# Performance work log

Hardware: AMD Instinct MI355X
Metric: run time of the kernel (lower is better)

## Reference

```python
import jax, jax.numpy as jnp
import numpy as np

C = 5.0          # tanh clamp constant (args.c, non-trainable)
B, N, R, D = 4, 16, 64, 256  # batch, block_num, block_len, word_dim
NEG = -1e9


def setup_inputs() -> dict:
    key = jax.random.key(0)
    ks = iter(jax.random.split(key, 80))

    def W(i, o):
        # xavier-like init (torch stores (out,in); we store (in,out) and use x @ W)
        return jax.random.normal(next(ks), (i, o), jnp.float32) * np.float32(np.sqrt(2.0 / (i + o)))

    def bvec(d):
        return jax.random.normal(next(ks), (d,), jnp.float32) * 0.01

    inp = {"x": jax.random.normal(next(ks), (B, N, R, D), jnp.float32)}
    for p in ("fw", "bw"):
        inp[f"fcW_{p}"] = W(D, D);  inp[f"fcb_{p}"] = bvec(D)
        inp[f"mW1_{p}"] = W(D, D);  inp[f"mW2_{p}"] = W(D, D);  inp[f"mb_{p}"] = bvec(D)
        inp[f"s2tW1_{p}"] = W(D, D); inp[f"s2tb1_{p}"] = bvec(D)
        inp[f"s2tW_{p}"] = W(D, D);  inp[f"s2tb_{p}"] = bvec(D)
        inp[f"gW1_{p}"] = W(D, D);  inp[f"gW2_{p}"] = W(D, D);  inp[f"gb_{p}"] = bvec(D)
        inp[f"fW1_{p}"] = W(3 * D, D); inp[f"fb1_{p}"] = bvec(D)
        inp[f"fW2_{p}"] = W(3 * D, D); inp[f"fb2_{p}"] = bvec(D)
    return inp


def _mSA(x, W1, W2, b, fw):
    # x: (..., L, d) -> (..., L, d). Additive per-feature attention with strict
    # triangular mask. fw: token i attends to j > i (last row zeroed);
    # bw: token i attends to j < i (first row zeroed). Matches the torch
    # -inf mask + narrow + zero-pad construction exactly.
    L = x.shape[-2]
    xi = (x @ W1)[..., :, None, :]                 # (..., L, 1, d)
    xj = (x @ W2)[..., None, :, :]                 # (..., 1, L, d)
    f = C * jnp.tanh((xi + xj + b) / C)            # (..., i, j, d)
    i = jnp.arange(L)[:, None]
    j = jnp.arange(L)[None, :]
    allowed = (j > i) if fw else (j < i)           # (L, L)
    scores = jnp.where(allowed[..., None], f, NEG)
    att = jax.nn.softmax(scores, axis=-2)          # softmax over j
    rowvalid = (jnp.arange(L) < L - 1) if fw else (jnp.arange(L) > 0)
    att = att * rowvalid[:, None, None].astype(x.dtype)
    return jnp.einsum('...ijd,...jd->...id', att, x)


def _s2t(x, W1, b1, Wo, bo):
    # source2token self-attention: (..., L, d) -> (..., d)
    f = jax.nn.relu(x @ W1 + b1)
    a = jax.nn.softmax(f @ Wo + bo, axis=-2)
    return jnp.sum(a * x, axis=-2)


def _mblosa(x, mW1, mW2, mb, s2tW1, s2tb1, s2tW, s2tb,
            gW1, gW2, gb, fW1, fb1, fW2, fb2, fw):
    Bb, n, r, d = x.shape
    h = _mSA(x, mW1, mW2, mb, fw)                  # (B, n, r, d) intra-block
    v = _s2t(h, s2tW1, s2tb1, s2tW, s2tb)          # (B, n, d)    block summary
    o = _mSA(v, mW1, mW2, mb, fw)                  # (B, n, d)    inter-block
    G = jax.nn.sigmoid(o @ gW1 + v @ gW2 + gb)
    e = G * o + (1.0 - G) * v                      # (B, n, d)
    # torch: cat of e[i] repeated r times, then narrow(1, 0, n)
    idx = jnp.arange(n) // r
    E = e[:, idx]                                  # (B, n, d)
    # torch: flatten blocks then narrow(1, 0, n) (faithful to source)
    xf = x.reshape(Bb, n * r, d)[:, :n]
    hf = h.reshape(Bb, n * r, d)[:, :n]
    cat = jnp.concatenate([xf, hf, E], axis=-1)    # (B, n, 3d)
    fusion = jax.nn.relu(cat @ fW1 + fb1)
    Gf = jax.nn.sigmoid(cat @ fW2 + fb2)
    return Gf * fusion + (1.0 - Gf) * xf           # (B, n, d)


def reference(x,
              fcW_fw, fcb_fw, mW1_fw, mW2_fw, mb_fw, s2tW1_fw, s2tb1_fw,
              s2tW_fw, s2tb_fw, gW1_fw, gW2_fw, gb_fw, fW1_fw, fb1_fw,
              fW2_fw, fb2_fw,
              fcW_bw, fcb_bw, mW1_bw, mW2_bw, mb_bw, s2tW1_bw, s2tb1_bw,
              s2tW_bw, s2tb_bw, gW1_bw, gW2_bw, gb_bw, fW1_bw, fb1_bw,
              fW2_bw, fb2_bw):
    in_fw = jax.nn.relu(x @ fcW_fw + fcb_fw)
    in_bw = jax.nn.relu(x @ fcW_bw + fcb_bw)
    u_fw = _mblosa(in_fw, mW1_fw, mW2_fw, mb_fw, s2tW1_fw, s2tb1_fw,
                   s2tW_fw, s2tb_fw, gW1_fw, gW2_fw, gb_fw,
                   fW1_fw, fb1_fw, fW2_fw, fb2_fw, True)
    u_bw = _mblosa(in_bw, mW1_bw, mW2_bw, mb_bw, s2tW1_bw, s2tb1_bw,
                   s2tW_bw, s2tb_bw, gW1_bw, gW2_bw, gb_bw,
                   fW1_bw, fb1_bw, fW2_bw, fb2_bw, False)
    return jnp.concatenate([u_fw, u_bw], axis=-1)  # (B, n, 2d)
```

## Files before the change

### kernel.cpp

```cpp
#include <hip/hip_runtime.h>
#include <hip/hip_bf16.h>

typedef __hip_bfloat16 BF16;
typedef __attribute__((ext_vector_type(8))) short short8;
typedef __attribute__((ext_vector_type(4))) short short4v;
typedef __attribute__((ext_vector_type(4))) float f32x4;

#define MFMA_B16(a,b,c) __builtin_amdgcn_mfma_f32_16x16x32_bf16((a),(b),(c),0,0,0)

#if __has_builtin(__builtin_amdgcn_exp2f)
#define EXP2F(x) __builtin_amdgcn_exp2f(x)
#else
#define EXP2F(x) __expf(0.6931471805599453f * (x))
#endif

__device__ __forceinline__ short f2bs(float f){ BF16 h = __float2bfloat16(f); return *(short*)&h; }
__device__ __forceinline__ float bs2f(short s){ BF16 h = *(BF16*)&s; return __bfloat162float(h); }

struct SrcPack { const float* s[10]; };

__global__ __launch_bounds__(256) void prep_k(SrcPack p, const float* __restrict__ X,
                                              short* __restrict__ Oh,
                                              short* __restrict__ Ol,
                                              short* __restrict__ Xh,
                                              short* __restrict__ Xl)
{
    if (blockIdx.y >= 10) {
        int u = (blockIdx.y - 10) * 16 + blockIdx.x;
        size_t base = (size_t)u * 16384;
        #pragma unroll
        for (int i = 0; i < 16; i++) {
            size_t idx = base + (size_t)i * 1024 + threadIdx.x * 4;
            float4 f = *(const float4*)(X + idx);
            short4v vh, vl;
            float t0[4] = {f.x, f.y, f.z, f.w};
            #pragma unroll
            for (int j = 0; j < 4; j++) {
                vh[j] = f2bs(t0[j]);
                vl[j] = f2bs(t0[j] - bs2f(vh[j]));
            }
            *(short4v*)(Xh + idx) = vh;
            *(short4v*)(Xl + idx) = vl;
        }
        return;
    }
    __shared__ float s[64][65];
    const float* W = p.s[blockIdx.y];
    short* oh = Oh + (size_t)blockIdx.y * 65536;
    short* ol = Ol + (size_t)blockIdx.y * 65536;
    int tr = (blockIdx.x >> 2) * 64, tc = (blockIdx.x & 3) * 64;
    #pragma unroll
    for (int i = 0; i < 16; i++) {
        int e = threadIdx.x + i * 256;
        int r = e >> 6, c = e & 63;
        s[c][r] = W[(size_t)(tr + r) * 256 + tc + c];
    }
    __syncthreads();
    #pragma unroll
    for (int i = 0; i < 16; i++) {
        int e = threadIdx.x + i * 256;
        int c2 = e >> 6, r2 = e & 63;
        float v = s[c2][r2];
        short hi = f2bs(v);
        short lo = f2bs(v - bs2f(hi));
        size_t oi = (size_t)(tc + c2) * 256 + tr + r2;
        oh[oi] = hi;
        ol[oi] = lo;
    }
}

template<int AM, int OM, int RELU, int BS>
__device__ __forceinline__ void gemm_body(const void* __restrict__ A0,
    const void* __restrict__ Alo,
    const short* __restrict__ Wh, const short* __restrict__ Wl,
    const float* __restrict__ bias, void* __restrict__ O0,
    int row0, int col0)
{
    constexpr int LDK = 72;
    __shared__ short sAh[64 * LDK];
    __shared__ short sAl[(AM == 0) ? 8 : 64 * LDK];
    __shared__ short sBh[64 * LDK];
    __shared__ short sBl[BS ? 8 : 64 * LDK];
    int tid = threadIdx.x;
    int w = tid >> 6, l = tid & 63;
    int m = l & 15, q = l >> 4;
    int sr = w * 16 + m;

    f32x4 acc[4];
    #pragma unroll
    for (int cf = 0; cf < 4; cf++) acc[cf] = (f32x4)(0.f);

    for (int kh = 0; kh < 4; kh++) {
        int kbase = kh * 64;
        #pragma unroll
        for (int i = 0; i < 2; i++) {
            int kl = q * 8 + 32 * i;
            size_t gofs = (size_t)(row0 + sr) * 256 + kbase + kl;
            if (AM == 2) {
                *(short8*)&sAh[sr * LDK + kl] = *(const short8*)((const short*)A0 + gofs);
                *(short8*)&sAl[sr * LDK + kl] = *(const short8*)((const short*)Alo + gofs);
            } else {
                *(short8*)&sAh[sr * LDK + kl] = *(const short8*)((const short*)A0 + gofs);
            }
            size_t gofsB = (size_t)(col0 + sr) * 256 + kbase + kl;
            *(short8*)&sBh[sr * LDK + kl] = *(const short8*)(Wh + gofsB);
            if (!BS)
                *(short8*)&sBl[sr * LDK + kl] = *(const short8*)(Wl + gofsB);
        }
        __syncthreads();
        #pragma unroll
        for (int ch = 0; ch < 2; ch++) {
            int k = ch * 32 + q * 8;
            short8 ah = *(const short8*)&sAh[(w * 16 + m) * LDK + k];
            short8 al = (AM != 0) ? *(const short8*)&sAl[(w * 16 + m) * LDK + k] : ah;
            #pragma unroll
            for (int cf = 0; cf < 4; cf++) {
                short8 bh = *(const short8*)&sBh[(cf * 16 + m) * LDK + k];
                acc[cf] = MFMA_B16(ah, bh, acc[cf]);
                if (!BS) {
                    short8 bl = *(const short8*)&sBl[(cf * 16 + m) * LDK + k];
                    acc[cf] = MFMA_B16(ah, bl, acc[cf]);
                }
                if (AM != 0)
                    acc[cf] = MFMA_B16(al, bh, acc[cf]);
            }
        }
        __syncthreads();
    }
    #pragma unroll
    for (int cf = 0; cf < 4; cf++) {
        int col = col0 + cf * 16 + m;
        float bv = bias ? bias[col] : 0.f;
        #pragma unroll
        for (int r = 0; r < 4; r++) {
            int row = row0 + w * 16 + q * 4 + r;
            float v = acc[cf][r] + bv;
            if (RELU) v = fmaxf(v, 0.f);
            size_t oi = (size_t)row * 256 + col;
            if (OM == 0) {
                ((float*)O0)[oi] = v;
            } else {
                ((short*)O0)[oi] = f2bs(v);
            }
        }
    }
}

struct GDir { const void* A0; const void* Al; const short* Wh; const short* Wl;
              const float* bias; void* O0; };

template<int AM, int OM, int RELU, int BS>
__global__ __launch_bounds__(256) void gemm_k(GDir p0, GDir p1)
{
    GDir p = blockIdx.z ? p1 : p0;
    gemm_body<AM, OM, RELU, BS>(p.A0, p.Al, p.Wh, p.Wl, p.bias, p.O0,
                                blockIdx.x * 64, blockIdx.y * 64);
}

struct MbloDir { const short* Ah;
                 const short* W1h; const short* W2h;
                 const float* mb; short* Hh; int fw; };

__global__ __launch_bounds__(512) void mblo_k(MbloDir p0, MbloDir p1)
{
    __shared__ char smraw[33536] __attribute__((aligned(16)));
    short* gAh  = (short*)smraw;
    short* gB1h = gAh + 4608;
    short* gB2h = gAh + 9216;
    float* aP   = (float*)smraw;
    unsigned int* aQX = (unsigned int*)(smraw + 16896);

    const float KLN = -0.06931471805599453f;

    MbloDir p = blockIdx.z ? p1 : p0;
    int tid = threadIdx.x;
    int w = tid >> 6, l = tid & 63;
    int m = l & 15, q = l >> 4;
    int rh = w >> 1;
    int cb = (w & 1) * 2;
    int bn = blockIdx.x >> 1, ipar = blockIdx.x & 1;
    int row0 = bn * 64, d0 = blockIdx.y * 64;
    int srow = tid >> 3;
    int skl  = (tid & 7) * 8;

    f32x4 acc1[2], acc2[2];
    #pragma unroll
    for (int cf = 0; cf < 2; cf++) { acc1[cf] = (f32x4)(0.f); acc2[cf] = (f32x4)(0.f); }

    for (int kh = 0; kh < 4; kh++) {
        int kbase = kh * 64;
        size_t ga = (size_t)(row0 + srow) * 256 + kbase + skl;
        *(short8*)&gAh[srow * 72 + skl] = *(const short8*)(p.Ah + ga);
        size_t gb = (size_t)(d0 + srow) * 256 + kbase + skl;
        *(short8*)&gB1h[srow * 72 + skl] = *(const short8*)(p.W1h + gb);
        *(short8*)&gB2h[srow * 72 + skl] = *(const short8*)(p.W2h + gb);
        __syncthreads();
        #pragma unroll
        for (int ch = 0; ch < 2; ch++) {
            int k = ch * 32 + q * 8;
            short8 ah = *(const short8*)&gAh[(rh * 16 + m) * 72 + k];
            #pragma unroll
            for (int cf = 0; cf < 2; cf++) {
                int bofs = ((cb + cf) * 16 + m) * 72 + k;
                short8 b1 = *(const short8*)&gB1h[bofs];
                acc1[cf] = MFMA_B16(ah, b1, acc1[cf]);
                short8 b2 = *(const short8*)&gB2h[bofs];
                acc2[cf] = MFMA_B16(ah, b2, acc2[cf]);
            }
        }
        __syncthreads();
    }
    short* sQX = (short*)aQX;
    #pragma unroll
    for (int cf = 0; cf < 2; cf++) {
        int col = (cb + cf) * 16 + m;
        float mbv = p.mb[d0 + col];
        #pragma unroll
        for (int r = 0; r < 4; r++) {
            int row = rh * 16 + q * 4 + r;
            aP[row * 66 + col] = __expf(0.4f * acc1[cf][r]) * KLN;
            sQX[col * 130 + 2 * row] = f2bs(__expf(0.4f * (acc2[cf][r] + mbv)));
        }
    }
    {
        size_t gx = (size_t)(row0 + srow) * 256 + d0 + skl;
        short8 xh = *(const short8*)(p.Ah + gx);
        #pragma unroll
        for (int t = 0; t < 8; t++)
            sQX[(skl + t) * 130 + 2 * srow + 1] = xh[t];
    }
    __syncthreads();
    const unsigned int* lane_qx = &aQX[l * 65];
    #pragma unroll
    for (int t8 = 0; t8 < 4; t8++) {
        int i = ipar + 2 * (w + 8 * t8);
        float Pp = aP[i * 66 + l];
        int js = p.fw ? (i + 1) : 0;
        int je = p.fw ? 64 : i;
        float den0 = 0.f, den1 = 0.f, num0 = 0.f, num1 = 0.f;
        int j = js;
        for (; j + 4 <= je; j += 4) {
            unsigned int u0 = lane_qx[j];
            unsigned int u1 = lane_qx[j + 1];
            unsigned int u2 = lane_qx[j + 2];
            unsigned int u3 = lane_qx[j + 3];
            float q0 = bs2f((short)(u0 & 0xffff)), x0 = bs2f((short)(u0 >> 16));
            float q1 = bs2f((short)(u1 & 0xffff)), x1 = bs2f((short)(u1 >> 16));
            float q2 = bs2f((short)(u2 & 0xffff)), x2 = bs2f((short)(u2 >> 16));
            float q3 = bs2f((short)(u3 & 0xffff)), x3 = bs2f((short)(u3 >> 16));
            float w0 = EXP2F(__builtin_amdgcn_rcpf(fmaf(Pp, q0, KLN)));
            float w1 = EXP2F(__builtin_amdgcn_rcpf(fmaf(Pp, q1, KLN)));
            float w2 = EXP2F(__builtin_amdgcn_rcpf(fmaf(Pp, q2, KLN)));
            float w3 = EXP2F(__builtin_amdgcn_rcpf(fmaf(Pp, q3, KLN)));
            den0 += w0; num0 = fmaf(w0, x0, num0);
            den1 += w1; num1 = fmaf(w1, x1, num1);
            den0 += w2; num0 = fmaf(w2, x2, num0);
            den1 += w3; num1 = fmaf(w3, x3, num1);
        }
        for (; j < je; j++) {
            unsigned int u0 = lane_qx[j];
            float q0 = bs2f((short)(u0 & 0xffff)), x0 = bs2f((short)(u0 >> 16));
            float wgt = EXP2F(__builtin_amdgcn_rcpf(fmaf(Pp, q0, KLN)));
            den0 += wgt; num0 = fmaf(wgt, x0, num0);
        }
        float den = den0 + den1, num = num0 + num1;
        bool valid = p.fw ? (i < 63) : (i > 0);
        float out = valid ? (num * __builtin_amdgcn_rcpf(den)) : 0.f;
        p.Hh[(size_t)(row0 + i) * 256 + d0 + l] = f2bs(out);
    }
}

struct PoolDir { const short* T1; const short* Wh; const float* bias;
                 const short* Hh; float* V; };

__global__ __launch_bounds__(256) void s2t_pool_k(PoolDir p0, PoolDir p1)
{
    __shared__ char smraw[37888] __attribute__((aligned(16)));
    short* gAh = (short*)smraw;
    short* gBh = gAh + 4608;
    float* aL = (float*)smraw;
    float* aH = aL + 4352;
    float* rm = aL + 8704;
    float* rd = aL + 8960;
    float* rn = aL + 9216;

    PoolDir p = blockIdx.z ? p1 : p0;
    int tid = threadIdx.x;
    int w = tid >> 6, l = tid & 63;
    int m = l & 15, q = l >> 4;
    int sr = w * 16 + m;
    int row0 = blockIdx.x * 64, d0 = blockIdx.y * 64;

    f32x4 acc[4];
    #pragma unroll
    for (int cf = 0; cf < 4; cf++) acc[cf] = (f32x4)(0.f);

    for (int kh = 0; kh < 4; kh++) {
        int kbase = kh * 64;
        #pragma unroll
        for (int i = 0; i < 2; i++) {
            int kl = q * 8 + 32 * i;
            *(short8*)&gAh[sr * 72 + kl] =
                *(const short8*)(p.T1 + (size_t)(row0 + sr) * 256 + kbase + kl);
            *(short8*)&gBh[sr * 72 + kl] =
                *(const short8*)(p.Wh + (size_t)(d0 + sr) * 256 + kbase + kl);
        }
        __syncthreads();
        #pragma unroll
        for (int ch = 0; ch < 2; ch++) {
            int k = ch * 32 + q * 8;
            short8 ah = *(const short8*)&gAh[(w * 16 + m) * 72 + k];
            #pragma unroll
            for (int cf = 0; cf < 4; cf++) {
                short8 bh = *(const short8*)&gBh[(cf * 16 + m) * 72 + k];
                acc[cf] = MFMA_B16(ah, bh, acc[cf]);
            }
        }
        __syncthreads();
    }
    #pragma unroll
    for (int cf = 0; cf < 4; cf++) {
        int col = cf * 16 + m;
        float bv = p.bias[d0 + col];
        #pragma unroll
        for (int r = 0; r < 4; r++) {
            int row = w * 16 + q * 4 + r;
            aL[row * 68 + col] = acc[cf][r] + bv;
        }
    }
    #pragma unroll
    for (int it = 0; it < 2; it++) {
        int e = tid + it * 256;
        int j = e >> 3, d8 = (e & 7) * 8;
        short8 xh = *(const short8*)(p.Hh + (size_t)(row0 + j) * 256 + d0 + d8);
        #pragma unroll
        for (int t = 0; t < 8; t++)
            aH[j * 68 + d8 + t] = bs2f(xh[t]);
    }
    __syncthreads();
    int dl = tid & 63, rq = tid >> 6;
    float mx = -1e30f, den = 0.f, num = 0.f;
    #pragma unroll
    for (int rr = 0; rr < 16; rr++) {
        int r = rq * 16 + rr;
        float lv = aL[r * 68 + dl];
        float hv = aH[r * 68 + dl];
        if (lv > mx) {
            float sc = __expf(mx - lv);
            den *= sc; num *= sc; mx = lv;
        }
        float wgt = __expf(lv - mx);
        den += wgt; num += wgt * hv;
    }
    rm[rq * 64 + dl] = mx; rd[rq * 64 + dl] = den; rn[rq * 64 + dl] = num;
    __syncthreads();
    if (rq == 0) {
        float M = fmaxf(fmaxf(rm[dl], rm[64 + dl]), fmaxf(rm[128 + dl], rm[192 + dl]));
        float D = 0.f, Nn = 0.f;
        #pragma unroll
        for (int k = 0; k < 4; k++) {
            float sc = __expf(rm[k * 64 + dl] - M);
            D += rd[k * 64 + dl] * sc;
            Nn += rn[k * 64 + dl] * sc;
        }
        p.V[(size_t)blockIdx.x * 256 + d0 + dl] = Nn / D;
    }
}

struct Gate2Dir { const float* V; const float* W1; const float* W2; const float* mb;
                  const float* gW1; const float* gW2; const float* gb;
                  float* E0; int fw; };

__global__ __launch_bounds__(512) void attn2gate_k(Gate2Dir p0, Gate2Dir p1)
{
    Gate2Dir p = blockIdx.z ? p1 : p0;
    __shared__ __attribute__((aligned(16))) float sVT[4096];
    __shared__ float sPart[16][256];
    __shared__ float so[256], sv[256], red[8][64];
    int tid = threadIdx.x;
    int b = blockIdx.x;
    int k = tid & 255, half = tid >> 8;

    if (p.fw) {
        #pragma unroll
        for (int it = 0; it < 8; it++) {
            int e = tid + it * 512;
            int kk = e >> 4, j = e & 15;
            sVT[e] = p.V[(size_t)(b * 16 + j) * 256 + kk];
        }
        __syncthreads();
        float acc[16];
        #pragma unroll
        for (int j = 0; j < 16; j++) acc[j] = 0.f;
        int kk0 = half * 128;
        #pragma unroll 4
        for (int kk = kk0; kk < kk0 + 128; kk++) {
            const float4* vr = (const float4*)&sVT[kk * 16];
            float4 va = vr[0], vb = vr[1], vc = vr[2], vd = vr[3];
            float w1 = p.W1[(size_t)kk * 256 + k];
            float w2 = p.W2[(size_t)kk * 256 + k];
            acc[0]  = fmaf(va.x, w1, acc[0]);
            acc[1]  = fmaf(va.y, w2, acc[1]);
            acc[2]  = fmaf(va.z, w2, acc[2]);
            acc[3]  = fmaf(va.w, w2, acc[3]);
            acc[4]  = fmaf(vb.x, w2, acc[4]);
            acc[5]  = fmaf(vb.y, w2, acc[5]);
            acc[6]  = fmaf(vb.z, w2, acc[6]);
            acc[7]  = fmaf(vb.w, w2, acc[7]);
            acc[8]  = fmaf(vc.x, w2, acc[8]);
            acc[9]  = fmaf(vc.y, w2, acc[9]);
            acc[10] = fmaf(vc.z, w2, acc[10]);
            acc[11] = fmaf(vc.w, w2, acc[11]);
            acc[12] = fmaf(vd.x, w2, acc[12]);
            acc[13] = fmaf(vd.y, w2, acc[13]);
            acc[14] = fmaf(vd.z, w2, acc[14]);
            acc[15] = fmaf(vd.w, w2, acc[15]);
        }
        if (half) {
            #pragma unroll
            for (int j = 0; j < 16; j++) sPart[j][k] = acc[j];
        }
        __syncthreads();
        if (!half) {
            #pragma unroll
            for (int j = 0; j < 16; j++) acc[j] += sPart[j][k];
            float base = acc[0] + p.mb[k];
            float den = 0.f, num = 0.f;
            #pragma unroll
            for (int j = 1; j < 16; j++) {
                float z = (base + acc[j]) * 0.2f;
                float e2 = __expf(2.f * z);
                float t = 1.f - 2.f / (e2 + 1.f);
                float wgt = __expf(5.f * t);
                den += wgt;
                num = fmaf(wgt, p.V[(size_t)(b * 16 + j) * 256 + k], num);
            }
            so[k] = num / den;
            sv[k] = p.V[(size_t)(b * 16) * 256 + k];
        }
    } else {
        if (!half) {
            so[k] = 0.f;
            sv[k] = p.V[(size_t)(b * 16) * 256 + k];
        }
    }
    __syncthreads();
    int c = tid & 63, ks = tid >> 6;
    int gc = blockIdx.y * 64 + c;
    float a2 = 0.f;
    int k0 = ks * 32;
    #pragma unroll 8
    for (int kkx = 0; kkx < 32; kkx++) {
        int kx = k0 + kkx;
        a2 += so[kx] * p.gW1[(size_t)kx * 256 + gc] + sv[kx] * p.gW2[(size_t)kx * 256 + gc];
    }
    red[ks][c] = a2;
    __syncthreads();
    if (ks == 0) {
        float a = red[0][c] + red[1][c] + red[2][c] + red[3][c]
                + red[4][c] + red[5][c] + red[6][c] + red[7][c] + p.gb[gc];
        float G = 1.f / (1.f + __expf(-a));
        p.E0[b * 256 + gc] = G * so[gc] + (1.f - G) * sv[gc];
    }
}

struct FuseDir { const short* INh; const short* Hh;
                 const float* E0; const float* fW1; const float* fb1;
                 const float* fW2; const float* fb2; };

__global__ __launch_bounds__(256) void fusion_k(FuseDir p0, FuseDir p1, float* __restrict__ out)
{
    FuseDir p = blockIdx.z ? p1 : p0;
    __shared__ float cat[768];
    __shared__ float red1[4][64], red2[4][64];
    int bt = blockIdx.x, b = bt >> 4, t = bt & 15;
    int c = threadIdx.x & 63, ks = threadIdx.x >> 6;
    int gc = blockIdx.y * 64 + c;
    size_t xrow = ((size_t)b * 1024 + t) * 256;
    cat[threadIdx.x]       = bs2f(p.INh[xrow + threadIdx.x]);
    cat[256 + threadIdx.x] = bs2f(p.Hh[xrow + threadIdx.x]);
    cat[512 + threadIdx.x] = p.E0[b * 256 + threadIdx.x];
    __syncthreads();
    float a1 = 0.f, a2 = 0.f;
    int k0 = ks * 192;
    #pragma unroll 8
    for (int kk = 0; kk < 192; kk++) {
        int k = k0 + kk;
        float cv = cat[k];
        a1 += cv * p.fW1[(size_t)k * 256 + gc];
        a2 += cv * p.fW2[(size_t)k * 256 + gc];
    }
    red1[ks][c] = a1; red2[ks][c] = a2;
    __syncthreads();
    if (ks == 0) {
        float s1 = red1[0][c] + red1[1][c] + red1[2][c] + red1[3][c] + p.fb1[gc];
        float s2 = red2[0][c] + red2[1][c] + red2[2][c] + red2[3][c] + p.fb2[gc];
        float fus = fmaxf(s1, 0.f);
        float Gf = 1.f / (1.f + __expf(-s2));
        float u = Gf * fus + (1.f - Gf) * cat[gc];
        out[((size_t)(b * 16 + t)) * 512 + (size_t)blockIdx.z * 256 + gc] = u;
    }
}

extern "C" void kernel_launch(void* const* d_in, const int* in_sizes, int n_in,
                              void* d_out, int out_size, void* d_ws, size_t ws_size,
                              hipStream_t stream)
{
    const float* x = (const float*)d_in[0];
    char* base = (char*)d_ws;
    auto alloc = [&](size_t bytes){ void* r = base; base += (bytes + 255) & ~255ULL; return r; };
    short* inH = (short*)alloc(2 * 1048576 * 2);
    short* hH  = (short*)alloc(2 * 1048576 * 2);
    short* t1  = (short*)alloc(2 * 1048576 * 2);
    short* wtH = (short*)alloc(10 * 65536 * 2);
    short* wtL = (short*)alloc(10 * 65536 * 2);
    short* xh  = (short*)alloc(1048576 * 2);
    short* xl  = (short*)alloc(1048576 * 2);
    float* v   = (float*)alloc(2 * 16384 * 4);
    float* E0  = (float*)alloc(2 * 1024 * 4);

    SrcPack sp;
    const int src_idx[5] = {0, 2, 3, 5, 7};
    for (int p = 0; p < 2; p++)
        for (int i = 0; i < 5; i++)
            sp.s[p * 5 + i] = (const float*)d_in[1 + p * 16 + src_idx[i]];
    prep_k<<<dim3(16, 14), 256, 0, stream>>>(sp, x, wtH, wtL, xh, xl);

    GDir fc[2], s2t1[2];
    MbloDir mbd[2];
    PoolDir pld[2];
    Gate2Dir gtd[2];
    FuseDir fsd[2];
    for (int p = 0; p < 2; p++) {
        int bi = 1 + p * 16;
        const float* fcb   = (const float*)d_in[bi + 1];
        const float* mb    = (const float*)d_in[bi + 4];
        const float* s2tb1 = (const float*)d_in[bi + 6];
        const float* s2tb  = (const float*)d_in[bi + 8];
        size_t po = (size_t)p * 1048576;
        const short* W0h = wtH + (size_t)(p * 5 + 0) * 65536, *W0l = wtL + (size_t)(p * 5 + 0) * 65536;
        const short* W1h = wtH + (size_t)(p * 5 + 1) * 65536;
        const short* W2h = wtH + (size_t)(p * 5 + 2) * 65536;
        const short* W3h = wtH + (size_t)(p * 5 + 3) * 65536;
        const short* W4h = wtH + (size_t)(p * 5 + 4) * 65536;

        fc[p]   = { xh, xl, W0h, W0l, fcb, inH + po };
        mbd[p]  = { inH + po, W1h, W2h, mb, hH + po, (p == 0) };
        s2t1[p] = { hH + po, nullptr, W3h, nullptr, s2tb1, t1 + po };
        pld[p]  = { t1 + po, W4h, s2tb, hH + po, v + p * 16384 };
        gtd[p]  = { v + p * 16384,
                    (const float*)d_in[bi + 2], (const float*)d_in[bi + 3], mb,
                    (const float*)d_in[bi + 9], (const float*)d_in[bi + 10],
                    (const float*)d_in[bi + 11], E0 + p * 1024, (p == 0) };
        fsd[p]  = { inH + po, hH + po, E0 + p * 1024,
                    (const float*)d_in[bi + 12], (const float*)d_in[bi + 13],
                    (const float*)d_in[bi + 14], (const float*)d_in[bi + 15] };
    }

    gemm_k<2, 1, 1, 0><<<dim3(64, 4, 2), 256, 0, stream>>>(fc[0], fc[1]);
    mblo_k<<<dim3(128, 4, 2), 512, 0, stream>>>(mbd[0], mbd[1]);
    gemm_k<0, 1, 1, 1><<<dim3(64, 4, 2), 256, 0, stream>>>(s2t1[0], s2t1[1]);
    s2t_pool_k<<<dim3(64, 4, 2), 256, 0, stream>>>(pld[0], pld[1]);
    attn2gate_k<<<dim3(4, 4, 2), 512, 0, stream>>>(gtd[0], gtd[1]);
    fusion_k<<<dim3(64, 4, 2), 256, 0, stream>>>(fsd[0], fsd[1], (float*)d_out);
}
```

Before: 211.4 us.

## Fuse all stages into one cooperative persistent kernel with grid syncs

```diff
diff --git a/kernel.cpp b/kernel.cpp
--- a/kernel.cpp
+++ b/kernel.cpp
@@ -1,4 +1,5 @@
 #include <hip/hip_runtime.h>
+#include <hip/hip_cooperative_groups.h>
 #include <hip/hip_bf16.h>
 
 typedef __hip_bfloat16 BF16;
@@ -18,6 +19,19 @@
 __device__ __forceinline__ float bs2f(short s){ BF16 h = *(BF16*)&s; return __bfloat162float(h); }
 
 struct SrcPack { const float* s[10]; };
+struct GDir { const void* A0; const void* Al; const short* Wh; const short* Wl;
+              const float* bias; void* O0; };
+struct MbloDir { const short* Ah; const short* W1h; const short* W2h;
+                 const float* mb; short* Hh; int fw; };
+struct PoolDir { const short* T1; const short* Wh; const float* bias;
+                 const short* Hh; float* V; };
+struct Gate2Dir { const float* V; const float* W1; const float* W2; const float* mb;
+                  const float* gW1; const float* gW2; const float* gb;
+                  float* E0; int fw; };
+struct FuseDir { const short* INh; const short* Hh;
+                 const float* E0; const float* fW1; const float* fb1;
+                 const float* fW2; const float* fb2; };
+
 
 __global__ __launch_bounds__(256) void prep_k(SrcPack p, const float* __restrict__ X,
                                               short* __restrict__ Oh,
@@ -146,9 +160,6 @@
     }
 }
 
-struct GDir { const void* A0; const void* Al; const short* Wh; const short* Wl;
-              const float* bias; void* O0; };
-
 template<int AM, int OM, int RELU, int BS>
 __global__ __launch_bounds__(256) void gemm_k(GDir p0, GDir p1)
 {
@@ -156,10 +167,6 @@
     gemm_body<AM, OM, RELU, BS>(p.A0, p.Al, p.Wh, p.Wl, p.bias, p.O0,
                                 blockIdx.x * 64, blockIdx.y * 64);
 }
-
-struct MbloDir { const short* Ah;
-                 const short* W1h; const short* W2h;
-                 const float* mb; short* Hh; int fw; };
 
 __global__ __launch_bounds__(512) void mblo_k(MbloDir p0, MbloDir p1)
 {
@@ -270,9 +277,6 @@
     }
 }
 
-struct PoolDir { const short* T1; const short* Wh; const float* bias;
-                 const short* Hh; float* V; };
-
 __global__ __launch_bounds__(256) void s2t_pool_k(PoolDir p0, PoolDir p1)
 {
     __shared__ char smraw[37888] __attribute__((aligned(16)));
@@ -366,10 +370,6 @@
         p.V[(size_t)blockIdx.x * 256 + d0 + dl] = Nn / D;
     }
 }
-
-struct Gate2Dir { const float* V; const float* W1; const float* W2; const float* mb;
-                  const float* gW1; const float* gW2; const float* gb;
-                  float* E0; int fw; };
 
 __global__ __launch_bounds__(512) void attn2gate_k(Gate2Dir p0, Gate2Dir p1)
 {
@@ -464,10 +464,6 @@
     }
 }
 
-struct FuseDir { const short* INh; const short* Hh;
-                 const float* E0; const float* fW1; const float* fb1;
-                 const float* fW2; const float* fb2; };
-
 __global__ __launch_bounds__(256) void fusion_k(FuseDir p0, FuseDir p1, float* __restrict__ out)
 {
     FuseDir p = blockIdx.z ? p1 : p0;
@@ -502,6 +498,481 @@
     }
 }
 
+
+struct MegaP {
+    SrcPack sp; const float* X;
+    short *wtH, *wtL, *xh, *xl;
+    GDir fc[2], s2t1[2];
+    MbloDir mbd[2];
+    PoolDir pld[2];
+    Gate2Dir gtd[2];
+    FuseDir fsd[2];
+    float* out;
+};
+
+template<int AM, int OM, int RELU, int BS>
+__device__ __forceinline__ void gemm512(const void* __restrict__ A0,
+    const void* __restrict__ Alo,
+    const short* __restrict__ Wh, const short* __restrict__ Wl,
+    const float* __restrict__ bias, void* __restrict__ O0,
+    int row0, int col0, char* SM)
+{
+    short* sAh = (short*)SM;
+    short* sAl = (short*)(SM + 9216);
+    short* sBh = (short*)(SM + 18432);
+    short* sBl = (short*)(SM + 27648);
+    int tid = threadIdx.x;
+    int w = tid >> 6, l = tid & 63, m = l & 15, q = l >> 4;
+    int strip = w >> 1, chalf = w & 1;
+    int srow = tid >> 3, skl = (tid & 7) * 8;
+    f32x4 acc[2];
+    acc[0] = (f32x4)(0.f); acc[1] = (f32x4)(0.f);
+    for (int kh = 0; kh < 4; kh++) {
+        int kb = kh * 64;
+        size_t ga = (size_t)(row0 + srow) * 256 + kb + skl;
+        *(short8*)&sAh[srow * 72 + skl] = *(const short8*)((const short*)A0 + ga);
+        if (AM == 2)
+            *(short8*)&sAl[srow * 72 + skl] = *(const short8*)((const short*)Alo + ga);
+        size_t gb = (size_t)(col0 + srow) * 256 + kb + skl;
+        *(short8*)&sBh[srow * 72 + skl] = *(const short8*)(Wh + gb);
+        if (!BS)
+            *(short8*)&sBl[srow * 72 + skl] = *(const short8*)(Wl + gb);
+        __syncthreads();
+        #pragma unroll
+        for (int ch = 0; ch < 2; ch++) {
+            int k = ch * 32 + q * 8;
+            short8 ah = *(const short8*)&sAh[(strip * 16 + m) * 72 + k];
+            short8 al = (AM == 2) ? *(const short8*)&sAl[(strip * 16 + m) * 72 + k] : ah;
+            #pragma unroll
+            for (int cf = 0; cf < 2; cf++) {
+                int bofs = ((chalf * 2 + cf) * 16 + m) * 72 + k;
+                short8 bh = *(const short8*)&sBh[bofs];
+                acc[cf] = MFMA_B16(ah, bh, acc[cf]);
+                if (!BS) {
+                    short8 bl = *(const short8*)&sBl[bofs];
+                    acc[cf] = MFMA_B16(ah, bl, acc[cf]);
+                }
+                if (AM == 2)
+                    acc[cf] = MFMA_B16(al, bh, acc[cf]);
+            }
+        }
+        __syncthreads();
+    }
+    #pragma unroll
+    for (int cf = 0; cf < 2; cf++) {
+        int col = col0 + (chalf * 2 + cf) * 16 + m;
+        float bv = bias ? bias[col] : 0.f;
+        #pragma unroll
+        for (int r = 0; r < 4; r++) {
+            int row = row0 + strip * 16 + q * 4 + r;
+            float v = acc[cf][r] + bv;
+            if (RELU) v = fmaxf(v, 0.f);
+            size_t oi = (size_t)row * 256 + col;
+            if (OM == 0) ((float*)O0)[oi] = v;
+            else ((short*)O0)[oi] = f2bs(v);
+        }
+    }
+}
+
+__global__ __launch_bounds__(512) void mega_k(MegaP mp)
+{
+    __shared__ char SM[40960] __attribute__((aligned(16)));
+    cooperative_groups::grid_group gg = cooperative_groups::this_grid();
+    const int tid = threadIdx.x;
+    const int bid = blockIdx.x, nb = gridDim.x;
+    const float KLN = -0.06931471805599453f;
+
+    for (int job = bid; job < 224; job += nb) {
+        if (job < 160) {
+            int mat = job >> 4, tile = job & 15;
+            float (*s)[65] = (float(*)[65])SM;
+            const float* W = mp.sp.s[mat];
+            short* oh = mp.wtH + (size_t)mat * 65536;
+            short* ol = mp.wtL + (size_t)mat * 65536;
+            int tr = (tile >> 2) * 64, tc = (tile & 3) * 64;
+            #pragma unroll
+            for (int i = 0; i < 8; i++) {
+                int e = tid + i * 512;
+                int r = e >> 6, c = e & 63;
+                s[c][r] = W[(size_t)(tr + r) * 256 + tc + c];
+            }
+            __syncthreads();
+            #pragma unroll
+            for (int i = 0; i < 8; i++) {
+                int e = tid + i * 512;
+                int c2 = e >> 6, r2 = e & 63;
+                float v = s[c2][r2];
+                short hi = f2bs(v);
+                short lo = f2bs(v - bs2f(hi));
+                size_t oi = (size_t)(tc + c2) * 256 + tr + r2;
+                oh[oi] = hi;
+                ol[oi] = lo;
+            }
+            __syncthreads();
+        } else {
+            int u = job - 160;
+            size_t base = (size_t)u * 16384;
+            #pragma unroll
+            for (int i = 0; i < 8; i++) {
+                size_t idx = base + (size_t)i * 2048 + tid * 4;
+                float4 f = *(const float4*)(mp.X + idx);
+                short4v vh, vl;
+                float t0[4] = {f.x, f.y, f.z, f.w};
+                #pragma unroll
+                for (int j = 0; j < 4; j++) {
+                    vh[j] = f2bs(t0[j]);
+                    vl[j] = f2bs(t0[j] - bs2f(vh[j]));
+                }
+                *(short4v*)(mp.xh + idx) = vh;
+                *(short4v*)(mp.xl + idx) = vl;
+            }
+        }
+    }
+    gg.sync();
+
+    for (int job = bid; job < 512; job += nb) {
+        int dir = job >> 8, rem = job & 255;
+        GDir p = mp.fc[dir];
+        gemm512<2, 1, 1, 0>(p.A0, p.Al, p.Wh, p.Wl, p.bias, p.O0,
+                            (rem & 63) * 64, (rem >> 6) * 64, SM);
+    }
+    gg.sync();
+
+    {
+        short* gAh  = (short*)SM;
+        short* gB1h = gAh + 4608;
+        short* gB2h = gAh + 9216;
+        float* aP   = (float*)SM;
+        unsigned int* aQX = (unsigned int*)(SM + 16896);
+        int w = tid >> 6, l = tid & 63, m = l & 15, q = l >> 4;
+        int rh = w >> 1, cb = (w & 1) * 2;
+        int srow = tid >> 3, skl = (tid & 7) * 8;
+        for (int job = bid; job < 512; job += nb) {
+            int dir = job >> 8, rem = job & 255;
+            MbloDir p = mp.mbd[dir];
+            int row0 = (rem & 63) * 64, d0 = (rem >> 6) * 64;
+            f32x4 acc1[2], acc2[2];
+            #pragma unroll
+            for (int cf = 0; cf < 2; cf++) { acc1[cf] = (f32x4)(0.f); acc2[cf] = (f32x4)(0.f); }
+            for (int kh = 0; kh < 4; kh++) {
+                int kbase = kh * 64;
+                size_t ga = (size_t)(row0 + srow) * 256 + kbase + skl;
+                *(short8*)&gAh[srow * 72 + skl] = *(const short8*)(p.Ah + ga);
+                size_t gb = (size_t)(d0 + srow) * 256 + kbase + skl;
+                *(short8*)&gB1h[srow * 72 + skl] = *(const short8*)(p.W1h + gb);
+                *(short8*)&gB2h[srow * 72 + skl] = *(const short8*)(p.W2h + gb);
+                __syncthreads();
+                #pragma unroll
+                for (int ch = 0; ch < 2; ch++) {
+                    int k = ch * 32 + q * 8;
+                    short8 ah = *(const short8*)&gAh[(rh * 16 + m) * 72 + k];
+                    #pragma unroll
+                    for (int cf = 0; cf < 2; cf++) {
+                        int bofs = ((cb + cf) * 16 + m) * 72 + k;
+                        short8 b1 = *(const short8*)&gB1h[bofs];
+                        acc1[cf] = MFMA_B16(ah, b1, acc1[cf]);
+                        short8 b2 = *(const short8*)&gB2h[bofs];
+                        acc2[cf] = MFMA_B16(ah, b2, acc2[cf]);
+                    }
+                }
+                __syncthreads();
+            }
+            short* sQX = (short*)aQX;
+            #pragma unroll
+            for (int cf = 0; cf < 2; cf++) {
+                int col = (cb + cf) * 16 + m;
+                float mbv = p.mb[d0 + col];
+                #pragma unroll
+                for (int r = 0; r < 4; r++) {
+                    int row = rh * 16 + q * 4 + r;
+                    aP[row * 66 + col] = __expf(0.4f * acc1[cf][r]) * KLN;
+                    sQX[col * 130 + 2 * row] = f2bs(__expf(0.4f * (acc2[cf][r] + mbv)));
+                }
+            }
+            {
+                size_t gx = (size_t)(row0 + srow) * 256 + d0 + skl;
+                short8 xh = *(const short8*)(p.Ah + gx);
+                #pragma unroll
+                for (int t = 0; t < 8; t++)
+                    sQX[(skl + t) * 130 + 2 * srow + 1] = xh[t];
+            }
+            __syncthreads();
+            const unsigned int* lane_qx = &aQX[l * 65];
+            for (int t8 = 0; t8 < 8; t8++) {
+                int i = w + 8 * t8;
+                float Pp = aP[i * 66 + l];
+                int js = p.fw ? (i + 1) : 0;
+                int je = p.fw ? 64 : i;
+                float den0 = 0.f, den1 = 0.f, num0 = 0.f, num1 = 0.f;
+                int j = js;
+                for (; j + 4 <= je; j += 4) {
+                    unsigned int u0 = lane_qx[j];
+                    unsigned int u1 = lane_qx[j + 1];
+                    unsigned int u2 = lane_qx[j + 2];
+                    unsigned int u3 = lane_qx[j + 3];
+                    float q0 = bs2f((short)(u0 & 0xffff)), x0 = bs2f((short)(u0 >> 16));
+                    float q1 = bs2f((short)(u1 & 0xffff)), x1 = bs2f((short)(u1 >> 16));
+                    float q2 = bs2f((short)(u2 & 0xffff)), x2 = bs2f((short)(u2 >> 16));
+                    float q3 = bs2f((short)(u3 & 0xffff)), x3 = bs2f((short)(u3 >> 16));
+                    float w0 = EXP2F(__builtin_amdgcn_rcpf(fmaf(Pp, q0, KLN)));
+                    float w1 = EXP2F(__builtin_amdgcn_rcpf(fmaf(Pp, q1, KLN)));
+                    float w2 = EXP2F(__builtin_amdgcn_rcpf(fmaf(Pp, q2, KLN)));
+                    float w3 = EXP2F(__builtin_amdgcn_rcpf(fmaf(Pp, q3, KLN)));
+                    den0 += w0; num0 = fmaf(w0, x0, num0);
+                    den1 += w1; num1 = fmaf(w1, x1, num1);
+                    den0 += w2; num0 = fmaf(w2, x2, num0);
+                    den1 += w3; num1 = fmaf(w3, x3, num1);
+                }
+                for (; j < je; j++) {
+                    unsigned int u0 = lane_qx[j];
+                    float q0 = bs2f((short)(u0 & 0xffff)), x0 = bs2f((short)(u0 >> 16));
+                    float wgt = EXP2F(__builtin_amdgcn_rcpf(fmaf(Pp, q0, KLN)));
+                    den0 += wgt; num0 = fmaf(wgt, x0, num0);
+                }
+                float den = den0 + den1, num = num0 + num1;
+                bool valid = p.fw ? (i < 63) : (i > 0);
+                float out = valid ? (num * __builtin_amdgcn_rcpf(den)) : 0.f;
+                p.Hh[(size_t)(row0 + i) * 256 + d0 + l] = f2bs(out);
+            }
+            __syncthreads();
+        }
+    }
+    gg.sync();
+
+    for (int job = bid; job < 512; job += nb) {
+        int dir = job >> 8, rem = job & 255;
+        GDir p = mp.s2t1[dir];
+        gemm512<0, 1, 1, 1>(p.A0, nullptr, p.Wh, nullptr, p.bias, p.O0,
+                            (rem & 63) * 64, (rem >> 6) * 64, SM);
+    }
+    gg.sync();
+
+    {
+        short* gAh = (short*)SM;
+        short* gBh = gAh + 4608;
+        float* aL = (float*)SM;
+        float* aH = aL + 4352;
+        float* rm = (float*)(SM + 34816);
+        float* rd = rm + 512;
+        float* rn = rm + 1024;
+        int w = tid >> 6, l = tid & 63, m = l & 15, q = l >> 4;
+        int strip = w >> 1, chalf = w & 1;
+        int srow = tid >> 3, skl = (tid & 7) * 8;
+        for (int job = bid; job < 512; job += nb) {
+            int dir = job >> 8, rem = job & 255;
+            PoolDir p = mp.pld[dir];
+            int row0 = (rem & 63) * 64, d0 = (rem >> 6) * 64;
+            f32x4 acc[2];
+            acc[0] = (f32x4)(0.f); acc[1] = (f32x4)(0.f);
+            for (int kh = 0; kh < 4; kh++) {
+                int kbase = kh * 64;
+                *(short8*)&gAh[srow * 72 + skl] =
+                    *(const short8*)(p.T1 + (size_t)(row0 + srow) * 256 + kbase + skl);
+                *(short8*)&gBh[srow * 72 + skl] =
+                    *(const short8*)(p.Wh + (size_t)(d0 + srow) * 256 + kbase + skl);
+                __syncthreads();
+                #pragma unroll
+                for (int ch = 0; ch < 2; ch++) {
+                    int k = ch * 32 + q * 8;
+                    short8 ah = *(const short8*)&gAh[(strip * 16 + m) * 72 + k];
+                    #pragma unroll
+                    for (int cf = 0; cf < 2; cf++) {
+                        short8 bh = *(const short8*)&gBh[((chalf * 2 + cf) * 16 + m) * 72 + k];
+                        acc[cf] = MFMA_B16(ah, bh, acc[cf]);
+                    }
+                }
+                __syncthreads();
+            }
+            #pragma unroll
+            for (int cf = 0; cf < 2; cf++) {
+                int col = (chalf * 2 + cf) * 16 + m;
+                float bv = p.bias[d0 + col];
+                #pragma unroll
+                for (int r = 0; r < 4; r++) {
+                    int row = strip * 16 + q * 4 + r;
+                    aL[row * 68 + col] = acc[cf][r] + bv;
+                }
+            }
+            {
+                int j = tid >> 3, d8 = (tid & 7) * 8;
+                short8 xh = *(const short8*)(p.Hh + (size_t)(row0 + j) * 256 + d0 + d8);
+                #pragma unroll
+                for (int t = 0; t < 8; t++)
+                    aH[j * 68 + d8 + t] = bs2f(xh[t]);
+            }
+            __syncthreads();
+            int dl = tid & 63, rq = tid >> 6;
+            float mx = -1e30f, den = 0.f, num = 0.f;
+            #pragma unroll
+            for (int rr = 0; rr < 8; rr++) {
+                int r = rq * 8 + rr;
+                float lv = aL[r * 68 + dl];
+                float hv = aH[r * 68 + dl];
+                if (lv > mx) { float sc = __expf(mx - lv); den *= sc; num *= sc; mx = lv; }
+                float wgt = __expf(lv - mx);
+                den += wgt; num = fmaf(wgt, hv, num);
+            }
+            rm[rq * 64 + dl] = mx; rd[rq * 64 + dl] = den; rn[rq * 64 + dl] = num;
+            __syncthreads();
+            if (rq == 0) {
+                float M = rm[dl];
+                #pragma unroll
+                for (int kq = 1; kq < 8; kq++) M = fmaxf(M, rm[kq * 64 + dl]);
+                float D = 0.f, Nn = 0.f;
+                #pragma unroll
+                for (int kq = 0; kq < 8; kq++) {
+                    float sc = __expf(rm[kq * 64 + dl] - M);
+                    D += rd[kq * 64 + dl] * sc;
+                    Nn += rn[kq * 64 + dl] * sc;
+                }
+                p.V[(size_t)(rem & 63) * 256 + d0 + dl] = Nn / D;
+            }
+            __syncthreads();
+        }
+    }
+    gg.sync();
+
+    {
+        float* sVT = (float*)SM;
+        float (*sPart)[256] = (float(*)[256])(SM + 16384);
+        float* so = (float*)(SM + 32768);
+        float* sv = (float*)(SM + 33792);
+        float (*red)[64] = (float(*)[64])(SM + 34816);
+        for (int job = bid; job < 32; job += nb) {
+            int b = job & 3, gy = (job >> 2) & 3, dir = job >> 4;
+            Gate2Dir p = mp.gtd[dir];
+            int k = tid & 255, half = tid >> 8;
+            if (p.fw) {
+                #pragma unroll
+                for (int it = 0; it < 8; it++) {
+                    int e = tid + it * 512;
+                    int kk = e >> 4, j = e & 15;
+                    sVT[e] = p.V[(size_t)(b * 16 + j) * 256 + kk];
+                }
+                __syncthreads();
+                float acc[16];
+                #pragma unroll
+                for (int j = 0; j < 16; j++) acc[j] = 0.f;
+                int kk0 = half * 128;
+                #pragma unroll 4
+                for (int kk = kk0; kk < kk0 + 128; kk++) {
+                    const float4* vr = (const float4*)&sVT[kk * 16];
+                    float4 va = vr[0], vb = vr[1], vc = vr[2], vd = vr[3];
+                    float w1 = p.W1[(size_t)kk * 256 + k];
+                    float w2 = p.W2[(size_t)kk * 256 + k];
+                    acc[0]  = fmaf(va.x, w1, acc[0]);
+                    acc[1]  = fmaf(va.y, w2, acc[1]);
+                    acc[2]  = fmaf(va.z, w2, acc[2]);
+                    acc[3]  = fmaf(va.w, w2, acc[3]);
+                    acc[4]  = fmaf(vb.x, w2, acc[4]);
+                    acc[5]  = fmaf(vb.y, w2, acc[5]);
+                    acc[6]  = fmaf(vb.z, w2, acc[6]);
+                    acc[7]  = fmaf(vb.w, w2, acc[7]);
+                    acc[8]  = fmaf(vc.x, w2, acc[8]);
+                    acc[9]  = fmaf(vc.y, w2, acc[9]);
+                    acc[10] = fmaf(vc.z, w2, acc[10]);
+                    acc[11] = fmaf(vc.w, w2, acc[11]);
+                    acc[12] = fmaf(vd.x, w2, acc[12]);
+                    acc[13] = fmaf(vd.y, w2, acc[13]);
+                    acc[14] = fmaf(vd.z, w2, acc[14]);
+                    acc[15] = fmaf(vd.w, w2, acc[15]);
+                }
+                if (half) {
+                    #pragma unroll
+                    for (int j = 0; j < 16; j++) sPart[j][k] = acc[j];
+                }
+                __syncthreads();
+                if (!half) {
+                    #pragma unroll
+                    for (int j = 0; j < 16; j++) acc[j] += sPart[j][k];
+                    float base = acc[0] + p.mb[k];
+                    float den = 0.f, num = 0.f;
+                    #pragma unroll
+                    for (int j = 1; j < 16; j++) {
+                        float z = (base + acc[j]) * 0.2f;
+                        float e2 = __expf(2.f * z);
+                        float t = 1.f - 2.f / (e2 + 1.f);
+                        float wgt = __expf(5.f * t);
+                        den += wgt;
+                        num = fmaf(wgt, p.V[(size_t)(b * 16 + j) * 256 + k], num);
+                    }
+                    so[k] = num / den;
+                    sv[k] = p.V[(size_t)(b * 16) * 256 + k];
+                }
+            } else {
+                if (!half) {
+                    so[k] = 0.f;
+                    sv[k] = p.V[(size_t)(b * 16) * 256 + k];
+                }
+            }
+            __syncthreads();
+            int c = tid & 63, ks = tid >> 6;
+            int gc = gy * 64 + c;
+            float a2 = 0.f;
+            int k0 = ks * 32;
+            #pragma unroll 8
+            for (int kkx = 0; kkx < 32; kkx++) {
+                int kx = k0 + kkx;
+                a2 += so[kx] * p.gW1[(size_t)kx * 256 + gc] + sv[kx] * p.gW2[(size_t)kx * 256 + gc];
+            }
+            red[ks][c] = a2;
+            __syncthreads();
+            if (ks == 0) {
+                float a = red[0][c] + red[1][c] + red[2][c] + red[3][c]
+                        + red[4][c] + red[5][c] + red[6][c] + red[7][c] + p.gb[gc];
+                float G = 1.f / (1.f + __expf(-a));
+                p.E0[b * 256 + gc] = G * so[gc] + (1.f - G) * sv[gc];
+            }
+            __syncthreads();
+        }
+    }
+    gg.sync();
+
+    {
+        float* cat = (float*)SM;
+        float (*red1)[64] = (float(*)[64])(SM + 3072);
+        float (*red2)[64] = (float(*)[64])(SM + 5120);
+        for (int job = bid; job < 512; job += nb) {
+            int dir = job >> 8, rem = job & 255;
+            int bt = rem & 63, gy = rem >> 6;
+            FuseDir p = mp.fsd[dir];
+            int b = bt >> 4, t = bt & 15;
+            size_t xrow = ((size_t)b * 1024 + t) * 256;
+            if (tid < 256) {
+                cat[tid] = bs2f(p.INh[xrow + tid]);
+                cat[512 + tid] = p.E0[b * 256 + tid];
+            } else {
+                cat[tid] = bs2f(p.Hh[xrow + tid - 256]);
+            }
+            __syncthreads();
+            int c = tid & 63, ks = tid >> 6;
+            int gc = gy * 64 + c;
+            float a1 = 0.f, a2 = 0.f;
+            int k0 = ks * 96;
+            #pragma unroll 8
+            for (int kk = 0; kk < 96; kk++) {
+                int k = k0 + kk;
+                float cv = cat[k];
+                a1 += cv * p.fW1[(size_t)k * 256 + gc];
+                a2 += cv * p.fW2[(size_t)k * 256 + gc];
+            }
+            red1[ks][c] = a1; red2[ks][c] = a2;
+            __syncthreads();
+            if (ks == 0) {
+                float s1 = p.fb1[gc], s2 = p.fb2[gc];
+                #pragma unroll
+                for (int kq = 0; kq < 8; kq++) { s1 += red1[kq][c]; s2 += red2[kq][c]; }
+                float fus = fmaxf(s1, 0.f);
+                float Gf = 1.f / (1.f + __expf(-s2));
+                float u = Gf * fus + (1.f - Gf) * cat[gc];
+                mp.out[((size_t)(b * 16 + t)) * 512 + (size_t)dir * 256 + gc] = u;
+            }
+            __syncthreads();
+        }
+    }
+}
+
+
 extern "C" void kernel_launch(void* const* d_in, const int* in_sizes, int n_in,
                               void* d_out, int out_size, void* d_ws, size_t ws_size,
                               hipStream_t stream)
@@ -524,7 +995,6 @@
     for (int p = 0; p < 2; p++)
         for (int i = 0; i < 5; i++)
             sp.s[p * 5 + i] = (const float*)d_in[1 + p * 16 + src_idx[i]];
-    prep_k<<<dim3(16, 14), 256, 0, stream>>>(sp, x, wtH, wtL, xh, xl);
 
     GDir fc[2], s2t1[2];
     MbloDir mbd[2];
@@ -557,10 +1027,47 @@
                     (const float*)d_in[bi + 14], (const float*)d_in[bi + 15] };
     }
 
-    gemm_k<2, 1, 1, 0><<<dim3(64, 4, 2), 256, 0, stream>>>(fc[0], fc[1]);
-    mblo_k<<<dim3(128, 4, 2), 512, 0, stream>>>(mbd[0], mbd[1]);
-    gemm_k<0, 1, 1, 1><<<dim3(64, 4, 2), 256, 0, stream>>>(s2t1[0], s2t1[1]);
-    s2t_pool_k<<<dim3(64, 4, 2), 256, 0, stream>>>(pld[0], pld[1]);
-    attn2gate_k<<<dim3(4, 4, 2), 512, 0, stream>>>(gtd[0], gtd[1]);
-    fusion_k<<<dim3(64, 4, 2), 256, 0, stream>>>(fsd[0], fsd[1], (float*)d_out);
+    static int coopGrid = -2;
+    if (coopGrid == -2) {
+        int perCU = 0;
+        hipError_t e1 = hipOccupancyMaxActiveBlocksPerMultiprocessor(&perCU, mega_k, 512, 0);
+        if (e1 == hipSuccess && perCU > 0) {
+            hipDeviceProp_t prop;
+            int dev = 0;
+            hipGetDevice(&dev);
+            if (hipGetDeviceProperties(&prop, dev) == hipSuccess && prop.cooperativeLaunch) {
+                long g = (long)perCU * prop.multiProcessorCount;
+                coopGrid = (int)(g > 512 ? 512 : g);
+            } else coopGrid = -1;
+        } else coopGrid = -1;
+    }
+
+    bool done = false;
+    if (coopGrid > 0) {
+        MegaP mp;
+        mp.sp = sp; mp.X = x;
+        mp.wtH = wtH; mp.wtL = wtL; mp.xh = xh; mp.xl = xl;
+        for (int p = 0; p < 2; p++) {
+            mp.fc[p] = fc[p]; mp.s2t1[p] = s2t1[p];
+            mp.mbd[p] = mbd[p]; mp.pld[p] = pld[p];
+            mp.gtd[p] = gtd[p]; mp.fsd[p] = fsd[p];
+        }
+        mp.out = (float*)d_out;
+        void* kargs[] = { (void*)&mp };
+        if (hipLaunchCooperativeKernel((void*)mega_k, dim3(coopGrid), dim3(512),
+                                       kargs, 0, stream) == hipSuccess)
+            done = true;
+        else
+            coopGrid = -1;
+    }
+
+    if (!done) {
+        prep_k<<<dim3(16, 14), 256, 0, stream>>>(sp, x, wtH, wtL, xh, xl);
+        gemm_k<2, 1, 1, 0><<<dim3(64, 4, 2), 256, 0, stream>>>(fc[0], fc[1]);
+        mblo_k<<<dim3(128, 4, 2), 512, 0, stream>>>(mbd[0], mbd[1]);
+        gemm_k<0, 1, 1, 1><<<dim3(64, 4, 2), 256, 0, stream>>>(s2t1[0], s2t1[1]);
+        s2t_pool_k<<<dim3(64, 4, 2), 256, 0, stream>>>(pld[0], pld[1]);
+        attn2gate_k<<<dim3(4, 4, 2), 512, 0, stream>>>(gtd[0], gtd[1]);
+        fusion_k<<<dim3(64, 4, 2), 256, 0, stream>>>(fsd[0], fsd[1], (float*)d_out);
+    }
 }
```

New measurement: 209.8 us. About the same (-0.8%).
